# Optimization experiments

Measured on AMD Instinct MI355X. Metric: run time of the kernel, lower is better.

Reference implementation:

```python
import jax, jax.numpy as jnp
import numpy as np

N_NODES = 50000
N_EDGES = 800000


def gat_conv(x, src, dst, ea, W, We, a_s, a_d, a_e, b, n_nodes):
    """PyG GATConv with edge_dim, add_self_loops=True, fill_value='mean', concat=True."""
    H, C = a_s.shape
    dt = x.dtype
    # self-loop edge_attr = mean of incoming edge attrs per destination node
    deg = jax.ops.segment_sum(jnp.ones((src.shape[0],), dt), dst, num_segments=n_nodes)
    loop_attr = jax.ops.segment_sum(ea, dst, num_segments=n_nodes) / jnp.clip(deg, 1.0)[:, None]
    nodes = jnp.arange(n_nodes, dtype=src.dtype)
    s = jnp.concatenate([src, nodes])
    d = jnp.concatenate([dst, nodes])
    e_attr = jnp.concatenate([ea, loop_attr], axis=0)       # [E2, edge_dim]
    h = (x @ W).reshape(n_nodes, H, C)                       # [N,H,C]
    e = (e_attr @ We).reshape(-1, H, C)                      # [E2,H,C]
    a_src = jnp.einsum('nhc,hc->nh', h, a_s)                 # [N,H]
    a_dst = jnp.einsum('nhc,hc->nh', h, a_d)
    a_edg = jnp.einsum('ehc,hc->eh', e, a_e)                 # [E2,H]
    lg = jax.nn.leaky_relu(a_src[s] + a_dst[d] + a_edg, 0.2)  # [E2,H]
    m = jax.ops.segment_max(lg, d, num_segments=n_nodes)     # every node has a self-loop
    p = jnp.exp(lg - m[d])
    z = jax.ops.segment_sum(p, d, num_segments=n_nodes)
    alpha = p / z[d]                                         # segment softmax over dst
    out = jax.ops.segment_sum(alpha[:, :, None] * h[s], d, num_segments=n_nodes)
    return out.reshape(n_nodes, H * C) + b


def setup_inputs() -> dict:
    key = jax.random.key(0)
    ks = iter(jax.random.split(key, 40))
    sc = 0.05
    inp = {
        'x': jax.random.normal(next(ks), (N_NODES, 128), jnp.float32),
        'edge_index': jax.random.randint(next(ks), (2, N_EDGES), 0, N_NODES, dtype=jnp.int32),
        'edge_attr': jax.random.uniform(next(ks), (N_EDGES, 1), jnp.float32),
        'fa_w': jax.random.normal(next(ks), (128, 128)) * sc, 'fa_b': jnp.zeros((128,)),
        'W1': jax.random.normal(next(ks), (128, 256)) * sc, 'We1': jax.random.normal(next(ks), (1, 256)) * sc,
        'as1': jax.random.normal(next(ks), (4, 64)) * sc, 'ad1': jax.random.normal(next(ks), (4, 64)) * sc,
        'ae1': jax.random.normal(next(ks), (4, 64)) * sc, 'b1': jnp.zeros((256,)),
        'W2': jax.random.normal(next(ks), (256, 256)) * sc, 'We2': jax.random.normal(next(ks), (1, 256)) * sc,
        'as2': jax.random.normal(next(ks), (4, 64)) * sc, 'ad2': jax.random.normal(next(ks), (4, 64)) * sc,
        'ae2': jax.random.normal(next(ks), (4, 64)) * sc, 'b2': jnp.zeros((256,)),
        'W3': jax.random.normal(next(ks), (256, 64)) * sc, 'We3': jax.random.normal(next(ks), (1, 64)) * sc,
        'as3': jax.random.normal(next(ks), (1, 64)) * sc, 'ad3': jax.random.normal(next(ks), (1, 64)) * sc,
        'ae3': jax.random.normal(next(ks), (1, 64)) * sc, 'b3': jnp.zeros((64,)),
        'r1_w': jax.random.normal(next(ks), (128, 256)) * sc, 'r1_b': jnp.zeros((256,)),
        'r2_w': jax.random.normal(next(ks), (256, 256)) * sc, 'r2_b': jnp.zeros((256,)),
        'ffn_w1': jax.random.normal(next(ks), (128, 64)) * sc, 'ffn_b1': jnp.zeros((64,)),
        'ffn_w2': jax.random.normal(next(ks), (64, 64)) * sc, 'ffn_b2': jnp.zeros((64,)),
    }
    return inp


def reference(x, edge_index, edge_attr, fa_w, fa_b,
              W1, We1, as1, ad1, ae1, b1,
              W2, We2, as2, ad2, ae2, b2,
              W3, We3, as3, ad3, ae3, b3,
              r1_w, r1_b, r2_w, r2_b,
              ffn_w1, ffn_b1, ffn_w2, ffn_b2):
    n = x.shape[0]
    src, dst = edge_index[0], edge_index[1]
    # feature attention gate
    x = x * jax.nn.sigmoid(x @ fa_w + fa_b)
    xr1 = x @ r1_w + r1_b
    z1 = gat_conv(x, src, dst, edge_attr, W1, We1, as1, ad1, ae1, b1, n)
    z1 = jax.nn.leaky_relu(z1, 0.01) + xr1          # dropout = identity (eval)
    z2 = gat_conv(z1, src, dst, edge_attr, W2, We2, as2, ad2, ae2, b2, n)
    z2 = jax.nn.leaky_relu(z2, 0.01) + (z1 @ r2_w + r2_b)
    z3 = gat_conv(z2, src, dst, edge_attr, W3, We3, as3, ad3, ae3, b3, n)
    z_self = jax.nn.relu(x @ ffn_w1 + ffn_b1) @ ffn_w2 + ffn_b2
    z3 = jax.nn.leaky_relu(z3, 0.01) + z_self
    return z3
```

## Files before the change

kernel.cpp:

```cpp
#include <hip/hip_runtime.h>
#include <hip/hip_bf16.h>


typedef unsigned short u16;
typedef unsigned int   u32;
typedef unsigned long long u64;
typedef __attribute__((ext_vector_type(8))) short short8;
typedef __attribute__((ext_vector_type(4))) float float4v;

typedef const __attribute__((address_space(1))) u32* gptr_t;
typedef __attribute__((address_space(3))) u32* lptr_t;
#define GLOAD_LDS16(g, l) \
    __builtin_amdgcn_global_load_lds((gptr_t)(const void*)(g), (lptr_t)(void*)(l), 16, 0, 0)

static __device__ __forceinline__ u16 f2b(float f) {
    u32 u = __float_as_uint(f);
    u32 r = u + 0x7fffu + ((u >> 16) & 1u);
    return (u16)(r >> 16);
}
static __device__ __forceinline__ float b2f(u16 u) {
    return __uint_as_float(((u32)u) << 16);
}
static __device__ __forceinline__ float lo2f(u32 v) { return __uint_as_float(v << 16); }
static __device__ __forceinline__ float hi2f(u32 v) { return __uint_as_float(v & 0xffff0000u); }
static __device__ __forceinline__ float lrelu02(float x) { return fmaxf(x, 0.2f * x); }

__global__ void prep_mega(const float* __restrict__ x, u16* __restrict__ xb, int n4,
                          const float* s0, const float* s1, const float* s2,
                          const float* s3, const float* s4, const float* s5,
                          const float* s6, const float* s7,
                          u16* d0, u16* d1, u16* d2, u16* d3,
                          u16* d4, u16* d5, u16* d6, u16* d7,
                          const float* We1, const float* ae1,
                          const float* We2, const float* ae2,
                          const float* We3, const float* ae3, float* ce_g,
                          const int* __restrict__ ei, const float* __restrict__ ea,
                          u64* packed, u32* rank, int E) {
    int role = blockIdx.y;
    if (role == 0) {
        int i = blockIdx.x * 256 + threadIdx.x;
        if (i >= n4) return;
        float4 v = ((const float4*)x)[i];
        ushort4 o;
        o.x = f2b(v.x); o.y = f2b(v.y); o.z = f2b(v.z); o.w = f2b(v.w);
        ((ushort4*)xb)[i] = o;
    } else if (role == 2) {
        int e = blockIdx.x * 256 + threadIdx.x;
        if (e >= E) return;
        int d = ei[E + e];
        u32 fx = (u32)__float2uint_rn(ea[e] * 16777216.0f);
        u64 ret = atomicAdd(&packed[d], (((u64)1) << 32) | (u64)fx);
        rank[e] = (u32)(ret >> 32);
    } else {
        int wid = blockIdx.x >> 4, sub = blockIdx.x & 15;
        if (wid > 8) return;
        if (wid == 8) {
            if (sub == 0) {
                int t = threadIdx.x;
                if (t < 9) {
                    const float* W; const float* a; int h;
                    if (t < 4)      { W = We1; a = ae1; h = t; }
                    else if (t < 8) { W = We2; a = ae2; h = t - 4; }
                    else            { W = We3; a = ae3; h = 0; }
                    float s = 0.f;
                    for (int c = 0; c < 64; c++) s += W[h * 64 + c] * a[h * 64 + c];
                    ce_g[t] = s;
                }
            }
            return;
        }
        const float* src; u16* dst; int K, N;
        switch (wid) {
            case 0: src = s0; dst = d0; K = 128; N = 128; break;
            case 1: src = s1; dst = d1; K = 128; N = 256; break;
            case 2: src = s2; dst = d2; K = 128; N = 256; break;
            case 3: src = s3; dst = d3; K = 256; N = 256; break;
            case 4: src = s4; dst = d4; K = 256; N = 256; break;
            case 5: src = s5; dst = d5; K = 256; N = 64;  break;
            case 6: src = s6; dst = d6; K = 128; N = 64;  break;
            default: src = s7; dst = d7; K = 64;  N = 64;  break;
        }
        int KN = K * N;
        int nmask = N - 1;
        int nshift = __popc((u32)nmask);
        for (int i = sub * 256 + threadIdx.x; i < KN; i += 16 * 256) {
            int k = i >> nshift, n2 = i & nmask;
            dst[(size_t)n2 * K + k] = f2b(src[i]);
        }
    }
}

__global__ void scan_block_kernel(const u64* __restrict__ packed, int* incl,
                                  int* blocksum, int Nn) {
    __shared__ int sb[256];
    int t = threadIdx.x;
    int n = blockIdx.x * 256 + t;
    int v = (n < Nn) ? (int)(packed[n] >> 32) : 0;
    sb[t] = v;
    __syncthreads();
    for (int off = 1; off < 256; off <<= 1) {
        int x = (t >= off) ? sb[t - off] : 0;
        __syncthreads();
        sb[t] += x;
        __syncthreads();
    }
    if (n < Nn) incl[n] = sb[t];
    if (t == 255) blocksum[blockIdx.x] = sb[255];
}

__global__ void scan_top_kernel(const int* __restrict__ blocksum, int* blockoff, int nb) {
    __shared__ int sb[256];
    int t = threadIdx.x;
    int v = (t < nb) ? blocksum[t] : 0;
    sb[t] = v;
    __syncthreads();
    for (int off = 1; off < 256; off <<= 1) {
        int x = (t >= off) ? sb[t - off] : 0;
        __syncthreads();
        sb[t] += x;
        __syncthreads();
    }
    if (t < nb) blockoff[t] = sb[t] - v;
}

__global__ void scan_final_kernel(const u64* __restrict__ packed, const int* __restrict__ incl,
                                  const int* __restrict__ blockoff,
                                  int* row_ptr, float* loop_attr, int Nn) {
    int n = blockIdx.x * 256 + threadIdx.x;
    if (n >= Nn) return;
    u64 pk = packed[n];
    int d = (int)(pk >> 32);
    float es = (float)((u32)pk) * (1.0f / 16777216.0f);
    int excl = blockoff[blockIdx.x] + incl[n] - d;
    row_ptr[n] = excl;
    if (n == Nn - 1) row_ptr[Nn] = excl + d;
    loop_attr[n] = es / (float)max(d, 1);
}

__global__ void scatter_kernel(const int* __restrict__ ei, const float* __restrict__ ea,
                               const int* __restrict__ row_ptr, const u32* __restrict__ rank,
                               int2* __restrict__ csr2, int E) {
    int e = blockIdx.x * 256 + threadIdx.x;
    if (e >= E) return;
    int d = ei[E + e];
    int pos = row_ptr[d] + (int)rank[e];
    csr2[pos] = make_int2(ei[e], __float_as_int(ea[e]));
}

template <int EPI, int K>
__global__ __launch_bounds__(256)
void gemm128_kernel(const u16* __restrict__ A, const u16* __restrict__ Bt,
                    const float* __restrict__ bias,
                    float* __restrict__ Cf, u16* __restrict__ Cb, int N) {
    __shared__ u16 As[128 * 32];
    __shared__ u16 Bs[128 * 32];
    int t = threadIdx.x;
    int w = t >> 6, lane = t & 63;
    int wm = w & 1, wn = w >> 1;
    int lm = lane & 15, q = lane >> 4;
    int bm = blockIdx.x * 128, bn = blockIdx.y * 128;

    float4v acc[4][4];
#pragma unroll
    for (int i = 0; i < 4; i++)
#pragma unroll
        for (int j = 0; j < 4; j++) acc[i][j] = (float4v){0.f, 0.f, 0.f, 0.f};

    int srow = lane >> 2;
    int scol = (lane & 3) * 8;
    const u16* aG = A + (size_t)(bm + w * 32 + srow) * K + scol;
    const u16* bG = Bt + (size_t)(bn + w * 32 + srow) * K + scol;
    u16* aL0 = &As[(w * 32) * 32];
    u16* aL1 = &As[(w * 32 + 16) * 32];
    u16* bL0 = &Bs[(w * 32) * 32];
    u16* bL1 = &Bs[(w * 32 + 16) * 32];

#pragma unroll
    for (int k0 = 0; k0 < K; k0 += 32) {
        GLOAD_LDS16(aG + k0, aL0);
        GLOAD_LDS16(aG + (size_t)16 * K + k0, aL1);
        GLOAD_LDS16(bG + k0, bL0);
        GLOAD_LDS16(bG + (size_t)16 * K + k0, bL1);
        __syncthreads();

        short8 af[4], bf[4];
#pragma unroll
        for (int i = 0; i < 4; i++)
            af[i] = *(const short8*)&As[(64 * wm + 16 * i + lm) * 32 + q * 8];
#pragma unroll
        for (int j = 0; j < 4; j++)
            bf[j] = *(const short8*)&Bs[(64 * wn + 16 * j + lm) * 32 + q * 8];
#pragma unroll
        for (int i = 0; i < 4; i++)
#pragma unroll
            for (int j = 0; j < 4; j++)
                acc[i][j] = __builtin_amdgcn_mfma_f32_16x16x32_bf16(af[i], bf[j], acc[i][j], 0, 0, 0);
        __syncthreads();
    }

#pragma unroll
    for (int i = 0; i < 4; i++)
#pragma unroll
        for (int j = 0; j < 4; j++) {
            int col = bn + 64 * wn + 16 * j + lm;
#pragma unroll
            for (int r = 0; r < 4; r++) {
                int row = bm + 64 * wm + 16 * i + q * 4 + r;
                float v = acc[i][j][r];
                if (EPI == 4) {
                    if (col < 256) {
                        v += bias[col];
                        Cf[(size_t)row * 256 + col] = v;
                    } else {
                        Cb[(size_t)row * 256 + (col - 256)] = f2b(v);
                    }
                } else {
                    Cb[(size_t)row * N + col] = f2b(v);
                }
            }
        }
}

template <int EPI, int K>
__global__ __launch_bounds__(256)
void gemm_kernel(const u16* __restrict__ A, const u16* __restrict__ Bt,
                 const float* __restrict__ bias, const u16* __restrict__ extraB,
                 float* __restrict__ Cf, u16* __restrict__ Cb, int N) {
#define LDSS 40
    __shared__ u16 As[64 * LDSS];
    __shared__ u16 Bs[64 * LDSS];
    int t = threadIdx.x;
    int bm = blockIdx.x * 64, bn = blockIdx.y * 64;
    int w = t >> 6, lane = t & 63;
    int wm = w & 1, wn = w >> 1;
    int lm = lane & 15, q = lane >> 4;

    float4v acc[2][2];
#pragma unroll
    for (int i = 0; i < 2; i++)
#pragma unroll
        for (int j = 0; j < 2; j++) acc[i][j] = (float4v){0.f, 0.f, 0.f, 0.f};

    int ar = t >> 2;
    int ac = (t & 3) * 8;
    const u16* aPtr = A + (size_t)(bm + ar) * K + ac;
    const u16* bPtr = Bt + (size_t)(bn + ar) * K + ac;

#pragma unroll
    for (int k0 = 0; k0 < K; k0 += 32) {
        uint4 av = *(const uint4*)(aPtr + k0);
        uint4 bv = *(const uint4*)(bPtr + k0);
        *(uint4*)&As[ar * LDSS + ac] = av;
        *(uint4*)&Bs[ar * LDSS + ac] = bv;
        __syncthreads();

        short8 fa0 = *(const short8*)&As[(32 * wm + lm) * LDSS + q * 8];
        short8 fa1 = *(const short8*)&As[(32 * wm + 16 + lm) * LDSS + q * 8];
        short8 fb0 = *(const short8*)&Bs[(32 * wn + lm) * LDSS + q * 8];
        short8 fb1 = *(const short8*)&Bs[(32 * wn + 16 + lm) * LDSS + q * 8];
        acc[0][0] = __builtin_amdgcn_mfma_f32_16x16x32_bf16(fa0, fb0, acc[0][0], 0, 0, 0);
        acc[0][1] = __builtin_amdgcn_mfma_f32_16x16x32_bf16(fa0, fb1, acc[0][1], 0, 0, 0);
        acc[1][0] = __builtin_amdgcn_mfma_f32_16x16x32_bf16(fa1, fb0, acc[1][0], 0, 0, 0);
        acc[1][1] = __builtin_amdgcn_mfma_f32_16x16x32_bf16(fa1, fb1, acc[1][1], 0, 0, 0);
        __syncthreads();
    }

#pragma unroll
    for (int i = 0; i < 2; i++)
#pragma unroll
        for (int j = 0; j < 2; j++) {
            int col = bn + 32 * wn + 16 * j + lm;
            float bval = (EPI >= 1) ? bias[col] : 0.f;
#pragma unroll
            for (int r = 0; r < 4; r++) {
                int row = bm + 32 * wm + 16 * i + q * 4 + r;
                float v = acc[i][j][r] + bval;
                if (EPI == 2) v = fmaxf(v, 0.f);
                if (EPI == 3) {
                    float xv = b2f(extraB[(size_t)row * N + col]);
                    v = xv / (1.f + __expf(-v));
                }
                size_t o = (size_t)row * N + col;
                if (EPI == 1) Cf[o] = v;
                else Cb[o] = f2b(v);
            }
        }
}

__global__ __launch_bounds__(256)
void att4_kernel(const uint2* __restrict__ hb2, const float* __restrict__ a_s,
                 const float* __restrict__ a_d, float* att_s, float* att_d, int Nn) {
    int wv = threadIdx.x >> 6;
    int n = blockIdx.x * 4 + wv;
    if (n >= Nn) return;
    int lane = threadIdx.x & 63;
    float4 as4 = *(const float4*)&a_s[lane * 4];
    float4 ad4 = *(const float4*)&a_d[lane * 4];
    uint2 v = hb2[(size_t)n * 64 + lane];
    float c0 = lo2f(v.x), c1 = hi2f(v.x), c2 = lo2f(v.y), c3 = hi2f(v.y);
    float ps = c0 * as4.x + c1 * as4.y + c2 * as4.z + c3 * as4.w;
    float pd = c0 * ad4.x + c1 * ad4.y + c2 * ad4.z + c3 * ad4.w;
#pragma unroll
    for (int off = 8; off > 0; off >>= 1) {
        ps += __shfl_down(ps, off);
        pd += __shfl_down(pd, off);
    }
    if ((lane & 15) == 0) {
        att_s[n * 4 + (lane >> 4)] = ps;
        att_d[n * 4 + (lane >> 4)] = pd;
    }
}

__global__ __launch_bounds__(256)
void att1_kernel(const u32* __restrict__ hb, const float* __restrict__ a_s,
                 const float* __restrict__ a_d, float* att_s, float* att_d, int Nn) {
    int wv = threadIdx.x >> 6;
    int n = blockIdx.x * 4 + wv;
    if (n >= Nn) return;
    int lane = threadIdx.x & 63;
    int cl = lane & 31;
    float2 as2 = *(const float2*)&a_s[cl * 2];
    float2 ad2 = *(const float2*)&a_d[cl * 2];
    u32 v = hb[(u32)n * 32u + cl];
    float c0 = lo2f(v), c1 = hi2f(v);
    float ps = c0 * as2.x + c1 * as2.y;
    float pd = c0 * ad2.x + c1 * ad2.y;
    if (lane >= 32) { ps = 0.f; pd = 0.f; }
#pragma unroll
    for (int off = 16; off > 0; off >>= 1) {
        ps += __shfl_down(ps, off);
        pd += __shfl_down(pd, off);
    }
    if (lane == 0) {
        att_s[n] = ps;
        att_d[n] = pd;
    }
}

__global__ __launch_bounds__(256)
void agg4_kernel(const uint2* __restrict__ hb2,
                 const float* __restrict__ att_s, const float* __restrict__ att_d,
                 const int* __restrict__ row_ptr, const int2* __restrict__ csr2,
                 const float* __restrict__ loop_attr,
                 const float* __restrict__ ce_g, const float* __restrict__ bias,
                 const float* __restrict__ resid, u16* __restrict__ outb, int Nn) {
    int wv = __builtin_amdgcn_readfirstlane(threadIdx.x >> 6);
    int n = blockIdx.x * 4 + wv;
    if (n >= Nn) return;
    int lane = threadIdx.x & 63;
    int hh = lane >> 4;

    float ce = ce_g[hh];
    float adn = att_d[n * 4 + hh];
    float lgs = lrelu02(att_s[n * 4 + hh] + adn + loop_attr[n] * ce);
    float zs = __expf(lgs);
    uint2 sv = hb2[(size_t)n * 64 + lane];
    float z = zs;
    float aA0 = zs * lo2f(sv.x), aA1 = zs * hi2f(sv.x);
    float aA2 = zs * lo2f(sv.y), aA3 = zs * hi2f(sv.y);
    float aB0 = 0.f, aB1 = 0.f, aB2 = 0.f, aB3 = 0.f;

    int e0 = row_ptr[n], e1 = row_ptr[n + 1];
    for (int base = e0; base < e1; base += 64) {
        int cnt = min(64, e1 - base);
        int2 cc = csr2[base + min(lane, cnt - 1)];
        int vsrc = cc.x;
        float vea = __int_as_float(cc.y);
        int i = 0;
        for (; i + 4 <= cnt; i += 4) {
            int sA = __shfl(vsrc, i);
            int sB = __shfl(vsrc, i + 1);
            int sC = __shfl(vsrc, i + 2);
            int sD = __shfl(vsrc, i + 3);
            float qA = __shfl(vea, i);
            float qB = __shfl(vea, i + 1);
            float qC = __shfl(vea, i + 2);
            float qD = __shfl(vea, i + 3);
            float gA = att_s[(u32)sA * 4u + hh];
            float gB = att_s[(u32)sB * 4u + hh];
            float gC = att_s[(u32)sC * 4u + hh];
            float gD = att_s[(u32)sD * 4u + hh];
            uint2 vA = hb2[(u32)sA * 64u + lane];
            uint2 vB = hb2[(u32)sB * 64u + lane];
            uint2 vC = hb2[(u32)sC * 64u + lane];
            uint2 vD = hb2[(u32)sD * 64u + lane];
            float pA = __expf(lrelu02(gA + adn + qA * ce));
            float pB = __expf(lrelu02(gB + adn + qB * ce));
            float pC = __expf(lrelu02(gC + adn + qC * ce));
            float pD = __expf(lrelu02(gD + adn + qD * ce));
            z += (pA + pB) + (pC + pD);
            aA0 = fmaf(pA, lo2f(vA.x), aA0); aA1 = fmaf(pA, hi2f(vA.x), aA1);
            aA2 = fmaf(pA, lo2f(vA.y), aA2); aA3 = fmaf(pA, hi2f(vA.y), aA3);
            aB0 = fmaf(pB, lo2f(vB.x), aB0); aB1 = fmaf(pB, hi2f(vB.x), aB1);
            aB2 = fmaf(pB, lo2f(vB.y), aB2); aB3 = fmaf(pB, hi2f(vB.y), aB3);
            aA0 = fmaf(pC, lo2f(vC.x), aA0); aA1 = fmaf(pC, hi2f(vC.x), aA1);
            aA2 = fmaf(pC, lo2f(vC.y), aA2); aA3 = fmaf(pC, hi2f(vC.y), aA3);
            aB0 = fmaf(pD, lo2f(vD.x), aB0); aB1 = fmaf(pD, hi2f(vD.x), aB1);
            aB2 = fmaf(pD, lo2f(vD.y), aB2); aB3 = fmaf(pD, hi2f(vD.y), aB3);
        }
        for (; i < cnt; i++) {
            int s = __shfl(vsrc, i);
            float q = __shfl(vea, i);
            float g = att_s[(u32)s * 4u + hh];
            uint2 v = hb2[(u32)s * 64u + lane];
            float p = __expf(lrelu02(g + adn + q * ce));
            z += p;
            aA0 = fmaf(p, lo2f(v.x), aA0); aA1 = fmaf(p, hi2f(v.x), aA1);
            aA2 = fmaf(p, lo2f(v.y), aA2); aA3 = fmaf(p, hi2f(v.y), aA3);
        }
    }
    float a0 = aA0 + aB0, a1 = aA1 + aB1, a2 = aA2 + aB2, a3 = aA3 + aB3;

    float inv = 1.f / z;
    int c0 = lane * 4;
    float4 bv = *(const float4*)&bias[c0];
    float4 rv = *(const float4*)&resid[(size_t)n * 256 + c0];
    float o0 = fmaf(a0, inv, bv.x);
    float o1 = fmaf(a1, inv, bv.y);
    float o2 = fmaf(a2, inv, bv.z);
    float o3 = fmaf(a3, inv, bv.w);
    o0 = fmaxf(o0, 0.01f * o0) + rv.x;
    o1 = fmaxf(o1, 0.01f * o1) + rv.y;
    o2 = fmaxf(o2, 0.01f * o2) + rv.z;
    o3 = fmaxf(o3, 0.01f * o3) + rv.w;
    uint2 packed;
    packed.x = ((u32)f2b(o0)) | (((u32)f2b(o1)) << 16);
    packed.y = ((u32)f2b(o2)) | (((u32)f2b(o3)) << 16);
    ((uint2*)outb)[(size_t)n * 64 + lane] = packed;
}

__global__ __launch_bounds__(256)
void agg1_kernel(const u32* __restrict__ hb,
                 const float* __restrict__ att_s, const float* __restrict__ att_d,
                 const int* __restrict__ row_ptr, const int2* __restrict__ csr2,
                 const float* __restrict__ loop_attr,
                 const float* __restrict__ ce_g, const float* __restrict__ bias,
                 const float* __restrict__ resid, float* __restrict__ outf, int Nn) {
    int wv = __builtin_amdgcn_readfirstlane(threadIdx.x >> 6);
    int n = blockIdx.x * 4 + wv;
    if (n >= Nn) return;
    int lane = threadIdx.x & 63;
    int par = lane >> 5;
    int cl = lane & 31;

    float ce = ce_g[8];
    float adn = att_d[n];
    float lgs = lrelu02(att_s[n] + adn + loop_attr[n] * ce);
    float zs = __expf(lgs);
    u32 sv = hb[(u32)n * 32u + cl];
    float z = (par == 0) ? zs : 0.f;
    float a0 = (par == 0) ? zs * lo2f(sv) : 0.f;
    float a1 = (par == 0) ? zs * hi2f(sv) : 0.f;

    int e0 = row_ptr[n], e1 = row_ptr[n + 1];
    for (int base = e0; base < e1; base += 64) {
        int cnt = min(64, e1 - base);
        int2 cc = csr2[base + min(lane, cnt - 1)];
        int vsrc = cc.x;
        float vea = __int_as_float(cc.y);
        for (int i = 0; i < cnt; i += 2) {
            int idx = min(i + par, cnt - 1);
            int s = __shfl(vsrc, idx);
            float q = __shfl(vea, idx);
            float p = __expf(lrelu02(att_s[s] + adn + q * ce));
            p = (i + par < cnt) ? p : 0.f;
            u32 v = hb[(u32)s * 32u + cl];
            z += p;
            a0 = fmaf(p, lo2f(v), a0);
            a1 = fmaf(p, hi2f(v), a1);
        }
    }
    z += __shfl_xor(z, 32);
    a0 += __shfl_xor(a0, 32);
    a1 += __shfl_xor(a1, 32);
    if (par == 0) {
        float inv = 1.f / z;
        int c0 = cl * 2;
        float2 bv = *(const float2*)&bias[c0];
        float2 rv = *(const float2*)&resid[(size_t)n * 64 + c0];
        float o0 = fmaf(a0, inv, bv.x);
        float o1 = fmaf(a1, inv, bv.y);
        o0 = fmaxf(o0, 0.01f * o0) + rv.x;
        o1 = fmaxf(o1, 0.01f * o1) + rv.y;
        *(float2*)&outf[(size_t)n * 64 + c0] = make_float2(o0, o1);
    }
}

extern "C" void kernel_launch(void* const* d_in, const int* in_sizes, int n_in,
                              void* d_out, int out_size, void* d_ws, size_t ws_size,
                              hipStream_t stream) {
    const float* x    = (const float*)d_in[0];
    const int*   ei   = (const int*)d_in[1];
    const float* ea   = (const float*)d_in[2];
    const float* fa_w = (const float*)d_in[3];
    const float* fa_b = (const float*)d_in[4];
    const float* W1   = (const float*)d_in[5];
    const float* We1  = (const float*)d_in[6];
    const float* as1  = (const float*)d_in[7];
    const float* ad1  = (const float*)d_in[8];
    const float* ae1  = (const float*)d_in[9];
    const float* b1   = (const float*)d_in[10];
    const float* W2   = (const float*)d_in[11];
    const float* We2  = (const float*)d_in[12];
    const float* as2  = (const float*)d_in[13];
    const float* ad2  = (const float*)d_in[14];
    const float* ae2  = (const float*)d_in[15];
    const float* b2   = (const float*)d_in[16];
    const float* W3   = (const float*)d_in[17];
    const float* We3  = (const float*)d_in[18];
    const float* as3  = (const float*)d_in[19];
    const float* ad3  = (const float*)d_in[20];
    const float* ae3  = (const float*)d_in[21];
    const float* b3   = (const float*)d_in[22];
    const float* r1_w = (const float*)d_in[23];
    const float* r1_b = (const float*)d_in[24];
    const float* r2_w = (const float*)d_in[25];
    const float* r2_b = (const float*)d_in[26];
    const float* fw1  = (const float*)d_in[27];
    const float* fb1  = (const float*)d_in[28];
    const float* fw2  = (const float*)d_in[29];
    const float* fb2  = (const float*)d_in[30];

    const int Nn = in_sizes[0] / 128;
    const int E  = in_sizes[1] / 2;

    char* ws = (char*)d_ws;
    size_t off = 0;
    auto alloc = [&](size_t bytes) -> char* {
        char* p = ws + off;
        off += (bytes + 255) & ~((size_t)255);
        return p;
    };
    u64*   packed   = (u64*)alloc((size_t)Nn * 8);
    u32*   rank     = (u32*)alloc((size_t)E * 4);
    int*   incl     = (int*)alloc((size_t)Nn * 4);
    int*   row_ptr  = (int*)alloc((size_t)(Nn + 1) * 4);
    int*   blocksum = (int*)alloc(1024);
    int*   blockoff = (int*)alloc(1024);
    float* lattr    = (float*)alloc((size_t)Nn * 4);
    float* att_s    = (float*)alloc((size_t)Nn * 16);
    float* att_d    = (float*)alloc((size_t)Nn * 16);
    int2*  csr2     = (int2*)alloc((size_t)E * 8);
    float* ce_g     = (float*)alloc(64);
    u16* xbf   = (u16*)alloc((size_t)(Nn + 128) * 128 * 2);
    u16* xg_bf = (u16*)alloc((size_t)(Nn + 128) * 128 * 2);
    u16* h_bf  = (u16*)alloc((size_t)(Nn + 128) * 256 * 2);
    u16* z_bf  = (u16*)alloc((size_t)(Nn + 128) * 256 * 2);
    u16* mid_bf = (u16*)alloc((size_t)(Nn + 128) * 64 * 2);
    u16* h3_bf  = (u16*)alloc((size_t)(Nn + 128) * 64 * 2);
    u16* wt_fa = (u16*)alloc(16384 * 2);
    u16* wt_c1 = (u16*)alloc((size_t)512 * 128 * 2);
    u16* wt_c2 = (u16*)alloc((size_t)512 * 256 * 2);
    u16* wt_W3 = (u16*)alloc(16384 * 2);
    u16* wt_f1 = (u16*)alloc(8192 * 2);
    u16* wt_f2 = (u16*)alloc(4096 * 2);
    float* residB = (float*)alloc((size_t)(Nn + 128) * 256 * 4);
    float* zself  = (float*)alloc((size_t)(Nn + 128) * 64 * 4);

    hipMemsetAsync(packed, 0, (size_t)Nn * 8, stream);

    int eb = (E + 255) / 256;
    int nb = (Nn + 255) / 256;
    int n4 = Nn * 128 / 4;
    int xb4 = (n4 + 255) / 256;

    prep_mega<<<dim3(max(xb4, eb), 3), 256, 0, stream>>>(
        x, xbf, n4,
        fa_w, r1_w, W1, r2_w, W2, W3, fw1, fw2,
        wt_fa, wt_c1, wt_c1 + (size_t)256 * 128, wt_c2, wt_c2 + (size_t)256 * 256,
        wt_W3, wt_f1, wt_f2, We1, ae1, We2, ae2, We3, ae3, ce_g,
        ei, ea, packed, rank, E);
    scan_block_kernel<<<nb, 256, 0, stream>>>(packed, incl, blocksum, Nn);
    scan_top_kernel<<<1, 256, 0, stream>>>(blocksum, blockoff, nb);
    scan_final_kernel<<<nb, 256, 0, stream>>>(packed, incl, blockoff, row_ptr, lattr, Nn);
    scatter_kernel<<<eb, 256, 0, stream>>>(ei, ea, row_ptr, rank, csr2, E);

    int mb  = (Nn + 63) / 64;
    int mb1 = (Nn + 127) / 128;
    int ab  = (Nn + 3) / 4;

    gemm_kernel<3, 128><<<dim3(mb, 2), 256, 0, stream>>>(xbf, wt_fa, fa_b, xbf, nullptr, xg_bf, 128);
    gemm128_kernel<4, 128><<<dim3(mb1, 4), 256, 0, stream>>>(xg_bf, wt_c1, r1_b, residB, h_bf, 512);
    att4_kernel<<<ab, 256, 0, stream>>>((const uint2*)h_bf, as1, ad1, att_s, att_d, Nn);
    agg4_kernel<<<ab, 256, 0, stream>>>((const uint2*)h_bf, att_s, att_d, row_ptr, csr2,
                                        lattr, ce_g, b1, residB, z_bf, Nn);
    gemm128_kernel<4, 256><<<dim3(mb1, 4), 256, 0, stream>>>(z_bf, wt_c2, r2_b, residB, h_bf, 512);
    att4_kernel<<<ab, 256, 0, stream>>>((const uint2*)h_bf, as2, ad2, att_s, att_d, Nn);
    agg4_kernel<<<ab, 256, 0, stream>>>((const uint2*)h_bf, att_s, att_d, row_ptr, csr2,
                                        lattr, ce_g + 4, b2, residB, z_bf, Nn);
    gemm_kernel<2, 128><<<dim3(mb, 1), 256, 0, stream>>>(xg_bf, wt_f1, fb1, nullptr, nullptr, mid_bf, 64);
    gemm_kernel<1, 64><<<dim3(mb, 1), 256, 0, stream>>>(mid_bf, wt_f2, fb2, nullptr, zself, nullptr, 64);
    gemm_kernel<0, 256><<<dim3(mb, 1), 256, 0, stream>>>(z_bf, wt_W3, nullptr, nullptr, nullptr, h3_bf, 64);
    att1_kernel<<<ab, 256, 0, stream>>>((const u32*)h3_bf, as3, ad3, att_s, att_d, Nn);
    agg1_kernel<<<ab, 256, 0, stream>>>((const u32*)h3_bf, att_s, att_d, row_ptr, csr2,
                                        lattr, ce_g, b3, zself, (float*)d_out, Nn);
}
```

Before: 504.3 us.

## Compute self-loop attr inside aggregation, drop packed atomics, merge scan kernels

The degree counting now uses 32-bit atomics instead of packed 64-bit atomics that also summed fixed-point edge attributes. The mean edge attribute for self-loops is computed inside the aggregation kernels from the CSR edges they already read, which removes the loop_attr array. The block-offset scan kernel is folded into the final scan kernel, where each block reduces the preceding block sums itself. The agg4 inner loop is unrolled to 8 edges for more memory-level parallelism, and agg1 is reorganised to process 4 edges per step with 16 lanes each using uint2 loads. The self-loop term is now added after the edge loop, so the computation order changes, and the extra shuffle reductions cost some work.

```diff
diff --git a/kernel.cpp b/kernel.cpp
--- a/kernel.cpp
+++ b/kernel.cpp
@@ -4,7 +4,6 @@
 
 typedef unsigned short u16;
 typedef unsigned int   u32;
-typedef unsigned long long u64;
 typedef __attribute__((ext_vector_type(8))) short short8;
 typedef __attribute__((ext_vector_type(4))) float float4v;
 
@@ -34,8 +33,8 @@
                           const float* We1, const float* ae1,
                           const float* We2, const float* ae2,
                           const float* We3, const float* ae3, float* ce_g,
-                          const int* __restrict__ ei, const float* __restrict__ ea,
-                          u64* packed, u32* rank, int E) {
+                          const int* __restrict__ ei,
+                          u32* deg, u32* rank, int E) {
     int role = blockIdx.y;
     if (role == 0) {
         int i = blockIdx.x * 256 + threadIdx.x;
@@ -48,9 +47,7 @@
         int e = blockIdx.x * 256 + threadIdx.x;
         if (e >= E) return;
         int d = ei[E + e];
-        u32 fx = (u32)__float2uint_rn(ea[e] * 16777216.0f);
-        u64 ret = atomicAdd(&packed[d], (((u64)1) << 32) | (u64)fx);
-        rank[e] = (u32)(ret >> 32);
+        rank[e] = atomicAdd(&deg[d], 1u);
     } else {
         int wid = blockIdx.x >> 4, sub = blockIdx.x & 15;
         if (wid > 8) return;
@@ -90,12 +87,12 @@
     }
 }
 
-__global__ void scan_block_kernel(const u64* __restrict__ packed, int* incl,
+__global__ void scan_block_kernel(const u32* __restrict__ deg, int* incl,
                                   int* blocksum, int Nn) {
     __shared__ int sb[256];
     int t = threadIdx.x;
     int n = blockIdx.x * 256 + t;
-    int v = (n < Nn) ? (int)(packed[n] >> 32) : 0;
+    int v = (n < Nn) ? (int)deg[n] : 0;
     sb[t] = v;
     __syncthreads();
     for (int off = 1; off < 256; off <<= 1) {
@@ -108,33 +105,25 @@
     if (t == 255) blocksum[blockIdx.x] = sb[255];
 }
 
-__global__ void scan_top_kernel(const int* __restrict__ blocksum, int* blockoff, int nb) {
+__global__ void scan_final_kernel(const u32* __restrict__ deg, const int* __restrict__ incl,
+                                  const int* __restrict__ blocksum,
+                                  int* row_ptr, int Nn) {
     __shared__ int sb[256];
     int t = threadIdx.x;
-    int v = (t < nb) ? blocksum[t] : 0;
-    sb[t] = v;
+    int b = blockIdx.x;
+    sb[t] = (t < b) ? blocksum[t] : 0;
     __syncthreads();
-    for (int off = 1; off < 256; off <<= 1) {
-        int x = (t >= off) ? sb[t - off] : 0;
+    for (int off = 128; off > 0; off >>= 1) {
+        if (t < off) sb[t] += sb[t + off];
         __syncthreads();
-        sb[t] += x;
-        __syncthreads();
-    }
-    if (t < nb) blockoff[t] = sb[t] - v;
-}
-
-__global__ void scan_final_kernel(const u64* __restrict__ packed, const int* __restrict__ incl,
-                                  const int* __restrict__ blockoff,
-                                  int* row_ptr, float* loop_attr, int Nn) {
-    int n = blockIdx.x * 256 + threadIdx.x;
+    }
+    int base = sb[0];
+    int n = b * 256 + t;
     if (n >= Nn) return;
-    u64 pk = packed[n];
-    int d = (int)(pk >> 32);
-    float es = (float)((u32)pk) * (1.0f / 16777216.0f);
-    int excl = blockoff[blockIdx.x] + incl[n] - d;
+    int d = (int)deg[n];
+    int excl = base + incl[n] - d;
     row_ptr[n] = excl;
     if (n == Nn - 1) row_ptr[Nn] = excl + d;
-    loop_attr[n] = es / (float)max(d, 1);
 }
 
 __global__ void scatter_kernel(const int* __restrict__ ei, const float* __restrict__ ea,
@@ -341,7 +330,6 @@
 void agg4_kernel(const uint2* __restrict__ hb2,
                  const float* __restrict__ att_s, const float* __restrict__ att_d,
                  const int* __restrict__ row_ptr, const int2* __restrict__ csr2,
-                 const float* __restrict__ loop_attr,
                  const float* __restrict__ ce_g, const float* __restrict__ bias,
                  const float* __restrict__ resid, u16* __restrict__ outb, int Nn) {
     int wv = __builtin_amdgcn_readfirstlane(threadIdx.x >> 6);
@@ -352,12 +340,10 @@
 
     float ce = ce_g[hh];
     float adn = att_d[n * 4 + hh];
-    float lgs = lrelu02(att_s[n * 4 + hh] + adn + loop_attr[n] * ce);
-    float zs = __expf(lgs);
+    float asn = att_s[n * 4 + hh];
     uint2 sv = hb2[(size_t)n * 64 + lane];
-    float z = zs;
-    float aA0 = zs * lo2f(sv.x), aA1 = zs * hi2f(sv.x);
-    float aA2 = zs * lo2f(sv.y), aA3 = zs * hi2f(sv.y);
+    float z = 0.f, qsum = 0.f;
+    float aA0 = 0.f, aA1 = 0.f, aA2 = 0.f, aA3 = 0.f;
     float aB0 = 0.f, aB1 = 0.f, aB2 = 0.f, aB3 = 0.f;
 
     int e0 = row_ptr[n], e1 = row_ptr[n + 1];
@@ -367,36 +353,49 @@
         int vsrc = cc.x;
         float vea = __int_as_float(cc.y);
         int i = 0;
-        for (; i + 4 <= cnt; i += 4) {
-            int sA = __shfl(vsrc, i);
-            int sB = __shfl(vsrc, i + 1);
-            int sC = __shfl(vsrc, i + 2);
-            int sD = __shfl(vsrc, i + 3);
-            float qA = __shfl(vea, i);
-            float qB = __shfl(vea, i + 1);
-            float qC = __shfl(vea, i + 2);
-            float qD = __shfl(vea, i + 3);
-            float gA = att_s[(u32)sA * 4u + hh];
-            float gB = att_s[(u32)sB * 4u + hh];
-            float gC = att_s[(u32)sC * 4u + hh];
-            float gD = att_s[(u32)sD * 4u + hh];
-            uint2 vA = hb2[(u32)sA * 64u + lane];
-            uint2 vB = hb2[(u32)sB * 64u + lane];
-            uint2 vC = hb2[(u32)sC * 64u + lane];
-            uint2 vD = hb2[(u32)sD * 64u + lane];
-            float pA = __expf(lrelu02(gA + adn + qA * ce));
-            float pB = __expf(lrelu02(gB + adn + qB * ce));
-            float pC = __expf(lrelu02(gC + adn + qC * ce));
-            float pD = __expf(lrelu02(gD + adn + qD * ce));
-            z += (pA + pB) + (pC + pD);
-            aA0 = fmaf(pA, lo2f(vA.x), aA0); aA1 = fmaf(pA, hi2f(vA.x), aA1);
-            aA2 = fmaf(pA, lo2f(vA.y), aA2); aA3 = fmaf(pA, hi2f(vA.y), aA3);
-            aB0 = fmaf(pB, lo2f(vB.x), aB0); aB1 = fmaf(pB, hi2f(vB.x), aB1);
-            aB2 = fmaf(pB, lo2f(vB.y), aB2); aB3 = fmaf(pB, hi2f(vB.y), aB3);
-            aA0 = fmaf(pC, lo2f(vC.x), aA0); aA1 = fmaf(pC, hi2f(vC.x), aA1);
-            aA2 = fmaf(pC, lo2f(vC.y), aA2); aA3 = fmaf(pC, hi2f(vC.y), aA3);
-            aB0 = fmaf(pD, lo2f(vD.x), aB0); aB1 = fmaf(pD, hi2f(vD.x), aB1);
-            aB2 = fmaf(pD, lo2f(vD.y), aB2); aB3 = fmaf(pD, hi2f(vD.y), aB3);
+        for (; i + 8 <= cnt; i += 8) {
+            int s0 = __shfl(vsrc, i),     s1 = __shfl(vsrc, i + 1);
+            int s2 = __shfl(vsrc, i + 2), s3 = __shfl(vsrc, i + 3);
+            int s4 = __shfl(vsrc, i + 4), s5 = __shfl(vsrc, i + 5);
+            int s6 = __shfl(vsrc, i + 6), s7 = __shfl(vsrc, i + 7);
+            float q0 = __shfl(vea, i),     q1 = __shfl(vea, i + 1);
+            float q2 = __shfl(vea, i + 2), q3 = __shfl(vea, i + 3);
+            float q4 = __shfl(vea, i + 4), q5 = __shfl(vea, i + 5);
+            float q6 = __shfl(vea, i + 6), q7 = __shfl(vea, i + 7);
+            float g0 = att_s[(u32)s0 * 4u + hh], g1 = att_s[(u32)s1 * 4u + hh];
+            float g2 = att_s[(u32)s2 * 4u + hh], g3 = att_s[(u32)s3 * 4u + hh];
+            float g4 = att_s[(u32)s4 * 4u + hh], g5 = att_s[(u32)s5 * 4u + hh];
+            float g6 = att_s[(u32)s6 * 4u + hh], g7 = att_s[(u32)s7 * 4u + hh];
+            uint2 v0 = hb2[(u32)s0 * 64u + lane], v1 = hb2[(u32)s1 * 64u + lane];
+            uint2 v2 = hb2[(u32)s2 * 64u + lane], v3 = hb2[(u32)s3 * 64u + lane];
+            uint2 v4 = hb2[(u32)s4 * 64u + lane], v5 = hb2[(u32)s5 * 64u + lane];
+            uint2 v6 = hb2[(u32)s6 * 64u + lane], v7 = hb2[(u32)s7 * 64u + lane];
+            float p0 = __expf(lrelu02(g0 + adn + q0 * ce));
+            float p1 = __expf(lrelu02(g1 + adn + q1 * ce));
+            float p2 = __expf(lrelu02(g2 + adn + q2 * ce));
+            float p3 = __expf(lrelu02(g3 + adn + q3 * ce));
+            float p4 = __expf(lrelu02(g4 + adn + q4 * ce));
+            float p5 = __expf(lrelu02(g5 + adn + q5 * ce));
+            float p6 = __expf(lrelu02(g6 + adn + q6 * ce));
+            float p7 = __expf(lrelu02(g7 + adn + q7 * ce));
+            qsum += ((q0 + q1) + (q2 + q3)) + ((q4 + q5) + (q6 + q7));
+            z += ((p0 + p1) + (p2 + p3)) + ((p4 + p5) + (p6 + p7));
+            aA0 = fmaf(p0, lo2f(v0.x), aA0); aA1 = fmaf(p0, hi2f(v0.x), aA1);
+            aA2 = fmaf(p0, lo2f(v0.y), aA2); aA3 = fmaf(p0, hi2f(v0.y), aA3);
+            aB0 = fmaf(p1, lo2f(v1.x), aB0); aB1 = fmaf(p1, hi2f(v1.x), aB1);
+            aB2 = fmaf(p1, lo2f(v1.y), aB2); aB3 = fmaf(p1, hi2f(v1.y), aB3);
+            aA0 = fmaf(p2, lo2f(v2.x), aA0); aA1 = fmaf(p2, hi2f(v2.x), aA1);
+            aA2 = fmaf(p2, lo2f(v2.y), aA2); aA3 = fmaf(p2, hi2f(v2.y), aA3);
+            aB0 = fmaf(p3, lo2f(v3.x), aB0); aB1 = fmaf(p3, hi2f(v3.x), aB1);
+            aB2 = fmaf(p3, lo2f(v3.y), aB2); aB3 = fmaf(p3, hi2f(v3.y), aB3);
+            aA0 = fmaf(p4, lo2f(v4.x), aA0); aA1 = fmaf(p4, hi2f(v4.x), aA1);
+            aA2 = fmaf(p4, lo2f(v4.y), aA2); aA3 = fmaf(p4, hi2f(v4.y), aA3);
+            aB0 = fmaf(p5, lo2f(v5.x), aB0); aB1 = fmaf(p5, hi2f(v5.x), aB1);
+            aB2 = fmaf(p5, lo2f(v5.y), aB2); aB3 = fmaf(p5, hi2f(v5.y), aB3);
+            aA0 = fmaf(p6, lo2f(v6.x), aA0); aA1 = fmaf(p6, hi2f(v6.x), aA1);
+            aA2 = fmaf(p6, lo2f(v6.y), aA2); aA3 = fmaf(p6, hi2f(v6.y), aA3);
+            aB0 = fmaf(p7, lo2f(v7.x), aB0); aB1 = fmaf(p7, hi2f(v7.x), aB1);
+            aB2 = fmaf(p7, lo2f(v7.y), aB2); aB3 = fmaf(p7, hi2f(v7.y), aB3);
         }
         for (; i < cnt; i++) {
             int s = __shfl(vsrc, i);
@@ -404,12 +403,19 @@
             float g = att_s[(u32)s * 4u + hh];
             uint2 v = hb2[(u32)s * 64u + lane];
             float p = __expf(lrelu02(g + adn + q * ce));
+            qsum += q;
             z += p;
             aA0 = fmaf(p, lo2f(v.x), aA0); aA1 = fmaf(p, hi2f(v.x), aA1);
             aA2 = fmaf(p, lo2f(v.y), aA2); aA3 = fmaf(p, hi2f(v.y), aA3);
         }
     }
-    float a0 = aA0 + aB0, a1 = aA1 + aB1, a2 = aA2 + aB2, a3 = aA3 + aB3;
+    float la = qsum / (float)max(e1 - e0, 1);
+    float ps = __expf(lrelu02(asn + adn + la * ce));
+    z += ps;
+    float a0 = aA0 + aB0 + ps * lo2f(sv.x);
+    float a1 = aA1 + aB1 + ps * hi2f(sv.x);
+    float a2 = aA2 + aB2 + ps * lo2f(sv.y);
+    float a3 = aA3 + aB3 + ps * hi2f(sv.y);
 
     float inv = 1.f / z;
     int c0 = lane * 4;
@@ -430,27 +436,24 @@
 }
 
 __global__ __launch_bounds__(256)
-void agg1_kernel(const u32* __restrict__ hb,
+void agg1_kernel(const uint2* __restrict__ hb2,
                  const float* __restrict__ att_s, const float* __restrict__ att_d,
                  const int* __restrict__ row_ptr, const int2* __restrict__ csr2,
-                 const float* __restrict__ loop_attr,
                  const float* __restrict__ ce_g, const float* __restrict__ bias,
                  const float* __restrict__ resid, float* __restrict__ outf, int Nn) {
     int wv = __builtin_amdgcn_readfirstlane(threadIdx.x >> 6);
     int n = blockIdx.x * 4 + wv;
     if (n >= Nn) return;
     int lane = threadIdx.x & 63;
-    int par = lane >> 5;
-    int cl = lane & 31;
+    int qtr = lane >> 4;
+    int cl = lane & 15;
 
     float ce = ce_g[8];
     float adn = att_d[n];
-    float lgs = lrelu02(att_s[n] + adn + loop_attr[n] * ce);
-    float zs = __expf(lgs);
-    u32 sv = hb[(u32)n * 32u + cl];
-    float z = (par == 0) ? zs : 0.f;
-    float a0 = (par == 0) ? zs * lo2f(sv) : 0.f;
-    float a1 = (par == 0) ? zs * hi2f(sv) : 0.f;
+    float asn = att_s[n];
+    uint2 sv = hb2[(u32)n * 16u + cl];
+    float z = 0.f, qsum = 0.f;
+    float a0 = 0.f, a1 = 0.f, a2 = 0.f, a3 = 0.f;
 
     int e0 = row_ptr[n], e1 = row_ptr[n + 1];
     for (int base = e0; base < e1; base += 64) {
@@ -458,31 +461,52 @@
         int2 cc = csr2[base + min(lane, cnt - 1)];
         int vsrc = cc.x;
         float vea = __int_as_float(cc.y);
-        for (int i = 0; i < cnt; i += 2) {
-            int idx = min(i + par, cnt - 1);
+        for (int i = 0; i < cnt; i += 4) {
+            int idx = min(i + qtr, cnt - 1);
             int s = __shfl(vsrc, idx);
             float q = __shfl(vea, idx);
+            bool act = (i + qtr < cnt);
             float p = __expf(lrelu02(att_s[s] + adn + q * ce));
-            p = (i + par < cnt) ? p : 0.f;
-            u32 v = hb[(u32)s * 32u + cl];
+            p = act ? p : 0.f;
+            q = act ? q : 0.f;
+            uint2 v = hb2[(u32)s * 16u + cl];
             z += p;
-            a0 = fmaf(p, lo2f(v), a0);
-            a1 = fmaf(p, hi2f(v), a1);
-        }
-    }
-    z += __shfl_xor(z, 32);
-    a0 += __shfl_xor(a0, 32);
-    a1 += __shfl_xor(a1, 32);
-    if (par == 0) {
+            qsum += q;
+            a0 = fmaf(p, lo2f(v.x), a0);
+            a1 = fmaf(p, hi2f(v.x), a1);
+            a2 = fmaf(p, lo2f(v.y), a2);
+            a3 = fmaf(p, hi2f(v.y), a3);
+        }
+    }
+    z += __shfl_xor(z, 16);      z += __shfl_xor(z, 32);
+    qsum += __shfl_xor(qsum, 16); qsum += __shfl_xor(qsum, 32);
+    a0 += __shfl_xor(a0, 16);    a0 += __shfl_xor(a0, 32);
+    a1 += __shfl_xor(a1, 16);    a1 += __shfl_xor(a1, 32);
+    a2 += __shfl_xor(a2, 16);    a2 += __shfl_xor(a2, 32);
+    a3 += __shfl_xor(a3, 16);    a3 += __shfl_xor(a3, 32);
+
+    float la = qsum / (float)max(e1 - e0, 1);
+    float ps = __expf(lrelu02(asn + adn + la * ce));
+    z += ps;
+    a0 += ps * lo2f(sv.x);
+    a1 += ps * hi2f(sv.x);
+    a2 += ps * lo2f(sv.y);
+    a3 += ps * hi2f(sv.y);
+
+    if (lane < 16) {
         float inv = 1.f / z;
-        int c0 = cl * 2;
-        float2 bv = *(const float2*)&bias[c0];
-        float2 rv = *(const float2*)&resid[(size_t)n * 64 + c0];
+        int c0 = cl * 4;
+        float4 bv = *(const float4*)&bias[c0];
+        float4 rv = *(const float4*)&resid[(size_t)n * 64 + c0];
         float o0 = fmaf(a0, inv, bv.x);
         float o1 = fmaf(a1, inv, bv.y);
+        float o2 = fmaf(a2, inv, bv.z);
+        float o3 = fmaf(a3, inv, bv.w);
         o0 = fmaxf(o0, 0.01f * o0) + rv.x;
         o1 = fmaxf(o1, 0.01f * o1) + rv.y;
-        *(float2*)&outf[(size_t)n * 64 + c0] = make_float2(o0, o1);
+        o2 = fmaxf(o2, 0.01f * o2) + rv.z;
+        o3 = fmaxf(o3, 0.01f * o3) + rv.w;
+        *(float4*)&outf[(size_t)n * 64 + c0] = make_float4(o0, o1, o2, o3);
     }
 }
 
@@ -531,13 +555,11 @@
         off += (bytes + 255) & ~((size_t)255);
         return p;
     };
-    u64*   packed   = (u64*)alloc((size_t)Nn * 8);
+    u32*   deg      = (u32*)alloc((size_t)Nn * 4);
     u32*   rank     = (u32*)alloc((size_t)E * 4);
     int*   incl     = (int*)alloc((size_t)Nn * 4);
     int*   row_ptr  = (int*)alloc((size_t)(Nn + 1) * 4);
     int*   blocksum = (int*)alloc(1024);
-    int*   blockoff = (int*)alloc(1024);
-    float* lattr    = (float*)alloc((size_t)Nn * 4);
     float* att_s    = (float*)alloc((size_t)Nn * 16);
     float* att_d    = (float*)alloc((size_t)Nn * 16);
     int2*  csr2     = (int2*)alloc((size_t)E * 8);
@@ -557,7 +579,7 @@
     float* residB = (float*)alloc((size_t)(Nn + 128) * 256 * 4);
     float* zself  = (float*)alloc((size_t)(Nn + 128) * 64 * 4);
 
-    hipMemsetAsync(packed, 0, (size_t)Nn * 8, stream);
+    hipMemsetAsync(deg, 0, (size_t)Nn * 4, stream);
 
     int eb = (E + 255) / 256;
     int nb = (Nn + 255) / 256;
@@ -569,10 +591,9 @@
         fa_w, r1_w, W1, r2_w, W2, W3, fw1, fw2,
         wt_fa, wt_c1, wt_c1 + (size_t)256 * 128, wt_c2, wt_c2 + (size_t)256 * 256,
         wt_W3, wt_f1, wt_f2, We1, ae1, We2, ae2, We3, ae3, ce_g,
-        ei, ea, packed, rank, E);
-    scan_block_kernel<<<nb, 256, 0, stream>>>(packed, incl, blocksum, Nn);
-    scan_top_kernel<<<1, 256, 0, stream>>>(blocksum, blockoff, nb);
-    scan_final_kernel<<<nb, 256, 0, stream>>>(packed, incl, blockoff, row_ptr, lattr, Nn);
+        ei, deg, rank, E);
+    scan_block_kernel<<<nb, 256, 0, stream>>>(deg, incl, blocksum, Nn);
+    scan_final_kernel<<<nb, 256, 0, stream>>>(deg, incl, blocksum, row_ptr, Nn);
     scatter_kernel<<<eb, 256, 0, stream>>>(ei, ea, row_ptr, rank, csr2, E);
 
     int mb  = (Nn + 63) / 64;
@@ -583,15 +604,15 @@
     gemm128_kernel<4, 128><<<dim3(mb1, 4), 256, 0, stream>>>(xg_bf, wt_c1, r1_b, residB, h_bf, 512);
     att4_kernel<<<ab, 256, 0, stream>>>((const uint2*)h_bf, as1, ad1, att_s, att_d, Nn);
     agg4_kernel<<<ab, 256, 0, stream>>>((const uint2*)h_bf, att_s, att_d, row_ptr, csr2,
-                                        lattr, ce_g, b1, residB, z_bf, Nn);
+                                        ce_g, b1, residB, z_bf, Nn);
     gemm128_kernel<4, 256><<<dim3(mb1, 4), 256, 0, stream>>>(z_bf, wt_c2, r2_b, residB, h_bf, 512);
     att4_kernel<<<ab, 256, 0, stream>>>((const uint2*)h_bf, as2, ad2, att_s, att_d, Nn);
     agg4_kernel<<<ab, 256, 0, stream>>>((const uint2*)h_bf, att_s, att_d, row_ptr, csr2,
-                                        lattr, ce_g + 4, b2, residB, z_bf, Nn);
+                                        ce_g + 4, b2, residB, z_bf, Nn);
     gemm_kernel<2, 128><<<dim3(mb, 1), 256, 0, stream>>>(xg_bf, wt_f1, fb1, nullptr, nullptr, mid_bf, 64);
     gemm_kernel<1, 64><<<dim3(mb, 1), 256, 0, stream>>>(mid_bf, wt_f2, fb2, nullptr, zself, nullptr, 64);
     gemm_kernel<0, 256><<<dim3(mb, 1), 256, 0, stream>>>(z_bf, wt_W3, nullptr, nullptr, nullptr, h3_bf, 64);
     att1_kernel<<<ab, 256, 0, stream>>>((const u32*)h3_bf, as3, ad3, att_s, att_d, Nn);
-    agg1_kernel<<<ab, 256, 0, stream>>>((const u32*)h3_bf, att_s, att_d, row_ptr, csr2,
-                                        lattr, ce_g, b3, zself, (float*)d_out, Nn);
-}
+    agg1_kernel<<<ab, 256, 0, stream>>>((const uint2*)h3_bf, att_s, att_d, row_ptr, csr2,
+                                        ce_g, b3, zself, (float*)d_out, Nn);
+}
```

Result: faster. 490.3 us (-2.8%).
